# Optimization experiments

Hardware: AMD Instinct MI355X
Metric: run time of the kernel (lower is better)

Reference implementation:

```python
import jax, jax.numpy as jnp
import numpy as np
from jax.scipy.linalg import expm

LAMBDA_ORTHO = 1.0


def setup_inputs() -> dict:
    key = jax.random.key(0)
    so8_raw = jax.random.normal(key, (524288, 8, 8), dtype=jnp.float32)
    return {"so8_raw": so8_raw}


def reference(so8_raw):
    # A = 0.5 * (P - P^T): skew-symmetric part per 8x8 block
    A = 0.5 * (so8_raw - jnp.swapaxes(so8_raw, -1, -2))
    # R = expm(A), batched over leading dim via vmap
    R = jax.vmap(expm)(A)
    # ||R^T R - I||_F per block, then mean over blocks
    gram = jnp.einsum('nji,njk->nik', R, R)  # R^T R, [N,8,8]
    err = gram - jnp.eye(8, dtype=R.dtype)
    ortho_err = jnp.sqrt(jnp.sum(err * err, axis=(1, 2))).mean()
    return LAMBDA_ORTHO * ortho_err
```

## Files before the change

### kernel.cpp

```cpp
#include <hip/hip_runtime.h>
#include <math.h>

#pragma clang fp contract(off)

typedef float f2 __attribute__((ext_vector_type(2)));

static __device__ __forceinline__ f2 sp(float x) { f2 r; r.x = x; r.y = x; return r; }
static __device__ __forceinline__ f2 sel2(bool d, f2 a, f2 b) {
  f2 r; r.x = d ? a.x : b.x; r.y = d ? a.y : b.y; return r;
}
#define FMA2(A, B, C) __builtin_elementwise_fma((A), (B), (C))

#define EL(m, i, j) (m[(i)*4 + ((j) >> 1)][(j) & 1])

#define UA(i, j) ((((i) * (15 - (i))) / 2) + (j) - (i) - 1)
#define ELA(i, k) ((i) < (k) ? ap[UA(i, k)] : ((i) > (k) ? -ap[UA(k, i)] : 0.0f))

__device__ __forceinline__ void mm8p(const f2* __restrict__ A,
                                     const f2* __restrict__ B,
                                     f2* __restrict__ C) {
  #pragma unroll
  for (int i = 0; i < 8; ++i) {
    #pragma unroll
    for (int c = 0; c < 4; ++c) {
      f2 s = sp(EL(A, i, 0)) * B[0*4 + c];
      #pragma unroll
      for (int k = 1; k < 8; ++k)
        s = FMA2(sp(EL(A, i, k)), B[k*4 + c], s);
      C[i*4 + c] = s;
    }
  }
}

__global__ __launch_bounds__(256, 1)
void triality_kernel(const float* __restrict__ in, double* __restrict__ acc)
{
  const int t = blockIdx.x * 256 + threadIdx.x;
  const float4* src = (const float4*)(in + (size_t)t * 64);

  float p[64];
  #pragma unroll
  for (int i = 0; i < 16; ++i) {
    float4 q4 = src[i];
    p[4*i+0] = q4.x; p[4*i+1] = q4.y; p[4*i+2] = q4.z; p[4*i+3] = q4.w;
  }

  float ap[28];
  #pragma unroll
  for (int i = 0; i < 8; ++i)
    #pragma unroll
    for (int j = i + 1; j < 8; ++j)
      ap[UA(i, j)] = 0.5f * (p[i*8 + j] - p[j*8 + i]);

  float l1 = 0.0f;
  #pragma unroll
  for (int j = 0; j < 8; ++j) {
    float cs = 0.0f;
    #pragma unroll
    for (int i = 0; i < 8; ++i) {
      if (i < j)      cs = cs + fabsf(ap[UA(i, j)]);
      else if (i > j) cs = cs + fabsf(ap[UA(j, i)]);
    }
    l1 = fmaxf(l1, cs);
  }

  float fl = floorf(log2f(l1 / 3.925724783138660f));
  int ns = (fl > 0.0f) ? (int)fl : 0;
  if (ns > 0) {
    float sc = exp2f((float)(-ns));
    #pragma unroll
    for (int m = 0; m < 28; ++m) ap[m] = ap[m] * sc;
  }

  f2 af[32];
  #pragma unroll
  for (int i = 0; i < 8; ++i)
    #pragma unroll
    for (int j = 0; j < 8; ++j)
      EL(af, i, j) = (i < j) ? ap[UA(i, j)]
                   : ((i > j) ? -ap[UA(j, i)] : 0.0f);

  f2 a2[32];
  #pragma unroll
  for (int i = 0; i < 8; ++i)
    #pragma unroll
    for (int c = 0; c < 4; ++c) {
      if (2*c + 1 >= i) {
        f2 s = sp(EL(af, i, 0)) * af[0*4 + c];
        #pragma unroll
        for (int k = 1; k < 8; ++k)
          s = FMA2(sp(EL(af, i, k)), af[k*4 + c], s);
        a2[i*4 + c] = s;
      }
    }
  #pragma unroll
  for (int i = 0; i < 8; ++i)
    #pragma unroll
    for (int c = 0; c < 4; ++c)
      if (2*c + 1 < i) {
        EL(a2, i, 2*c)     = EL(a2, 2*c,     i);
        EL(a2, i, 2*c + 1) = EL(a2, 2*c + 1, i);
      }

  f2 a4[32];
  #pragma unroll
  for (int i = 0; i < 8; ++i)
    #pragma unroll
    for (int c = 0; c < 4; ++c) {
      if (2*c + 1 >= i) {
        f2 s = sp(EL(a2, i, 0)) * a2[0*4 + c];
        #pragma unroll
        for (int k = 1; k < 8; ++k)
          s = FMA2(sp(EL(a2, i, k)), a2[k*4 + c], s);
        a4[i*4 + c] = s;
      }
    }
  #pragma unroll
  for (int i = 0; i < 8; ++i)
    #pragma unroll
    for (int c = 0; c < 4; ++c)
      if (2*c + 1 < i) {
        EL(a4, i, 2*c)     = EL(a4, 2*c,     i);
        EL(a4, i, 2*c + 1) = EL(a4, 2*c + 1, i);
      }

  f2 w6[32];
  #pragma unroll
  for (int i = 0; i < 8; ++i)
    #pragma unroll
    for (int c = 0; c < 4; ++c) {
      f2 s = sp(EL(a4, i, 0)) * a2[0*4 + c];
      #pragma unroll
      for (int k = 1; k < 8; ++k)
        s = FMA2(sp(EL(a4, i, k)), a2[k*4 + c], s);
      w6[i*4 + c] = s;
    }

  f2 vv[32];
  #pragma unroll
  for (int e = 0; e < 32; ++e) {
    f2 x6 = w6[e], x4 = a4[e], x2 = a2[e];
    f2 w = FMA2(sp(1512.0f), x4, x6);
    w = FMA2(sp(277200.0f), x2, w);
    f2 v = FMA2(sp(56.0f), x6, sp(25200.0f) * x4);
    v = FMA2(sp(1995840.0f), x2, v);
    w6[e] = w; vv[e] = v;
  }
  #pragma unroll
  for (int i = 0; i < 8; ++i) {
    EL(w6, i, i) = EL(w6, i, i) + 8648640.0f;
    EL(vv, i, i) = EL(vv, i, i) + 17297280.0f;
  }

  f2 uu[32];
  #pragma unroll
  for (int i = 0; i < 8; ++i)
    #pragma unroll
    for (int c = 0; c < 4; ++c) {
      f2 s = sp(ELA(i, 0)) * w6[0*4 + c];
      #pragma unroll
      for (int k = 1; k < 8; ++k)
        s = FMA2(sp(ELA(i, k)), w6[k*4 + c], s);
      f2 V = vv[i*4 + c];
      uu[i*4 + c] = s + V;
      vv[i*4 + c] = V - s;
    }
  f2* P = uu;
  f2* Q = vv;

  #pragma unroll
  for (int k = 0; k < 8; ++k) {
    float amax = fabsf(EL(Q, k, k)); int jp = k;
    #pragma unroll
    for (int i = k + 1; i < 8; ++i) {
      float av = fabsf(EL(Q, i, k));
      if (av > amax) { amax = av; jp = i; }
    }
    const int c0 = k >> 1;
    #pragma unroll
    for (int i = k + 1; i < 8; ++i) {
      bool d = (jp == i);
      #pragma unroll
      for (int c = c0; c < 4; ++c) {
        f2 qk = Q[k*4 + c], qi = Q[i*4 + c];
        Q[k*4 + c] = sel2(d, qi, qk);
        Q[i*4 + c] = sel2(d, qk, qi);
      }
      #pragma unroll
      for (int c = 0; c < 4; ++c) {
        f2 pk_ = P[k*4 + c], pi = P[i*4 + c];
        P[k*4 + c] = sel2(d, pi, pk_);
        P[i*4 + c] = sel2(d, pk_, pi);
      }
    }

    float dk = EL(Q, k, k);
    #pragma unroll
    for (int i = k + 1; i < 8; ++i) EL(Q, i, k) = EL(Q, i, k) / dk;
    #pragma unroll
    for (int i = k + 1; i < 8; ++i) {
      float lik = EL(Q, i, k);
      f2 nl = sp(-lik);
      #pragma unroll
      for (int c = c0; c < 4; ++c)
        Q[i*4 + c] = FMA2(nl, Q[k*4 + c], Q[i*4 + c]);
      #pragma unroll
      for (int c = 0; c < 4; ++c)
        P[i*4 + c] = FMA2(nl, P[k*4 + c], P[i*4 + c]);
    }
  }

  #pragma unroll
  for (int k = 7; k >= 0; --k) {
    float dk = EL(Q, k, k);
    #pragma unroll
    for (int j = 0; j < 8; ++j) EL(P, k, j) = EL(P, k, j) / dk;
    #pragma unroll
    for (int i = 0; i < k; ++i) {
      f2 nu = sp(-EL(Q, i, k));
      #pragma unroll
      for (int c = 0; c < 4; ++c)
        P[i*4 + c] = FMA2(nu, P[k*4 + c], P[i*4 + c]);
    }
  }

  for (int sq = 0; sq < ns; ++sq) {
    f2 t2[32];
    mm8p(P, P, t2);
    #pragma unroll
    for (int e = 0; e < 32; ++e) P[e] = t2[e];
  }

  f2 s2p = sp(0.0f);
  #pragma unroll
  for (int i = 0; i < 8; ++i) {
    #pragma unroll
    for (int c = 0; c < 4; ++c) {
      if (2*c + 1 >= i) {
        f2 g = sp(EL(P, 0, i)) * P[0*4 + c];
        #pragma unroll
        for (int j = 1; j < 8; ++j)
          g = FMA2(sp(EL(P, j, i)), P[j*4 + c], g);
        f2 idv; idv.x = (2*c == i) ? 1.0f : 0.0f;
        idv.y = (2*c + 1 == i) ? 1.0f : 0.0f;
        f2 e = g - idv;
        f2 we;
        we.x = (2*c > i) ? (e.x + e.x) : ((2*c == i) ? e.x : 0.0f);
        we.y = (2*c + 1 == i) ? e.y : (e.y + e.y);
        s2p = FMA2(we, e, s2p);
      }
    }
  }
  float frob = sqrtf(s2p.x + s2p.y);

  double dv = (double)frob;
  #pragma unroll
  for (int off = 32; off > 0; off >>= 1)
    dv += __shfl_down(dv, off);

  __shared__ double part[4];
  const int lane = threadIdx.x & 63;
  const int wid  = threadIdx.x >> 6;
  if (lane == 0) part[wid] = dv;
  __syncthreads();
  if (threadIdx.x == 0) {
    double s = (part[0] + part[1]) + (part[2] + part[3]);
    atomicAdd(acc, s);
  }
}

__global__ void finalize_kernel(const double* __restrict__ acc,
                                float* __restrict__ out, int nmat)
{
  out[0] = (float)(acc[0] / (double)nmat);
}

extern "C" void kernel_launch(void* const* d_in, const int* in_sizes, int n_in,
                              void* d_out, int out_size, void* d_ws, size_t ws_size,
                              hipStream_t stream) {
  const float* in = (const float*)d_in[0];
  float* out = (float*)d_out;
  double* acc = (double*)d_ws;
  int nmat = in_sizes[0] / 64;
  hipMemsetAsync(d_ws, 0, sizeof(double), stream);
  triality_kernel<<<nmat / 256, 256, 0, stream>>>(in, acc);
  finalize_kernel<<<1, 1, 0, stream>>>(acc, out, nmat);
}
```

Baseline: 248.1 us.

## Pack symmetric A^4 and reuse buffers to cut registers for two blocks per CU

Stores A^4 as a packed 36-entry upper triangle computed with scalar FMAs instead of a full 8x8 f2 matrix. The vv and uu buffers are replaced by reusing a2 in place, and the U·W product is reordered column-major. Launch bounds go from 1 to 2 blocks per CU so the lower register footprint can raise occupancy. The risk is spilling if the compiler cannot fit the budget, and scalar FMAs replace packed ones for A^4.

```diff
diff --git a/kernel.cpp b/kernel.cpp
--- a/kernel.cpp
+++ b/kernel.cpp
@@ -14,6 +14,8 @@
 #define EL(m, i, j) (m[(i)*4 + ((j) >> 1)][(j) & 1])
 
 #define UA(i, j) ((((i) * (15 - (i))) / 2) + (j) - (i) - 1)
+#define U4(i, j) ((((i) * (17 - (i))) / 2) + (j) - (i))
+#define A4P(i, k) ((i) <= (k) ? a4p[U4(i, k)] : a4p[U4(k, i)])
 #define ELA(i, k) ((i) < (k) ? ap[UA(i, k)] : ((i) > (k) ? -ap[UA(k, i)] : 0.0f))
 
 __device__ __forceinline__ void mm8p(const f2* __restrict__ A,
@@ -32,7 +34,7 @@
   }
 }
 
-__global__ __launch_bounds__(256, 1)
+__global__ __launch_bounds__(256, 2)
 void triality_kernel(const float* __restrict__ in, double* __restrict__ acc)
 {
   const int t = blockIdx.x * 256 + threadIdx.x;
@@ -102,71 +104,64 @@
         EL(a2, i, 2*c + 1) = EL(a2, 2*c + 1, i);
       }
 
-  f2 a4[32];
-  #pragma unroll
-  for (int i = 0; i < 8; ++i)
-    #pragma unroll
-    for (int c = 0; c < 4; ++c) {
-      if (2*c + 1 >= i) {
-        f2 s = sp(EL(a2, i, 0)) * a2[0*4 + c];
-        #pragma unroll
-        for (int k = 1; k < 8; ++k)
-          s = FMA2(sp(EL(a2, i, k)), a2[k*4 + c], s);
-        a4[i*4 + c] = s;
-      }
-    }
-  #pragma unroll
-  for (int i = 0; i < 8; ++i)
-    #pragma unroll
-    for (int c = 0; c < 4; ++c)
-      if (2*c + 1 < i) {
-        EL(a4, i, 2*c)     = EL(a4, 2*c,     i);
-        EL(a4, i, 2*c + 1) = EL(a4, 2*c + 1, i);
-      }
+  float a4p[36];
+  #pragma unroll
+  for (int i = 0; i < 8; ++i)
+    #pragma unroll
+    for (int j = i; j < 8; ++j) {
+      float s = EL(a2, i, 0) * EL(a2, 0, j);
+      #pragma unroll
+      for (int k = 1; k < 8; ++k)
+        s = __builtin_fmaf(EL(a2, i, k), EL(a2, k, j), s);
+      a4p[U4(i, j)] = s;
+    }
 
   f2 w6[32];
   #pragma unroll
   for (int i = 0; i < 8; ++i)
     #pragma unroll
     for (int c = 0; c < 4; ++c) {
-      f2 s = sp(EL(a4, i, 0)) * a2[0*4 + c];
-      #pragma unroll
-      for (int k = 1; k < 8; ++k)
-        s = FMA2(sp(EL(a4, i, k)), a2[k*4 + c], s);
+      f2 s = sp(A4P(i, 0)) * a2[0*4 + c];
+      #pragma unroll
+      for (int k = 1; k < 8; ++k)
+        s = FMA2(sp(A4P(i, k)), a2[k*4 + c], s);
       w6[i*4 + c] = s;
     }
 
-  f2 vv[32];
-  #pragma unroll
-  for (int e = 0; e < 32; ++e) {
-    f2 x6 = w6[e], x4 = a4[e], x2 = a2[e];
-    f2 w = FMA2(sp(1512.0f), x4, x6);
-    w = FMA2(sp(277200.0f), x2, w);
-    f2 v = FMA2(sp(56.0f), x6, sp(25200.0f) * x4);
-    v = FMA2(sp(1995840.0f), x2, v);
-    w6[e] = w; vv[e] = v;
-  }
+  #pragma unroll
+  for (int i = 0; i < 8; ++i)
+    #pragma unroll
+    for (int c = 0; c < 4; ++c) {
+      f2 x2 = a2[i*4 + c], x6 = w6[i*4 + c];
+      f2 x4; x4.x = A4P(i, 2*c); x4.y = A4P(i, 2*c + 1);
+      f2 w = FMA2(sp(1512.0f), x4, x6);
+      w = FMA2(sp(277200.0f), x2, w);
+      f2 v = FMA2(sp(56.0f), x6, sp(25200.0f) * x4);
+      v = FMA2(sp(1995840.0f), x2, v);
+      w6[i*4 + c] = w;
+      a2[i*4 + c] = v;
+    }
   #pragma unroll
   for (int i = 0; i < 8; ++i) {
     EL(w6, i, i) = EL(w6, i, i) + 8648640.0f;
-    EL(vv, i, i) = EL(vv, i, i) + 17297280.0f;
-  }
-
-  f2 uu[32];
-  #pragma unroll
-  for (int i = 0; i < 8; ++i)
-    #pragma unroll
-    for (int c = 0; c < 4; ++c) {
+    EL(a2, i, i) = EL(a2, i, i) + 17297280.0f;
+  }
+
+  f2 pp[32];
+  #pragma unroll
+  for (int c = 0; c < 4; ++c)
+    #pragma unroll
+    for (int i = 0; i < 8; ++i) {
       f2 s = sp(ELA(i, 0)) * w6[0*4 + c];
       #pragma unroll
       for (int k = 1; k < 8; ++k)
         s = FMA2(sp(ELA(i, k)), w6[k*4 + c], s);
-      f2 V = vv[i*4 + c];
-      uu[i*4 + c] = s + V;
-      vv[i*4 + c] = V - s;
-    }
-  f2* P = uu;
-  f2* Q = vv;
+      f2 V = a2[i*4 + c];
+      pp[i*4 + c] = s + V;
+      a2[i*4 + c] = V - s;
+    }
+  f2* P = pp;
+  f2* Q = a2;
 
   #pragma unroll
   for (int k = 0; k < 8; ++k) {
```

Result: no change. 249.5 us (+0.6%).
